# Kernel optimization log

Hardware: AMD Instinct MI355X
Metric: run time of the kernel (lower is better)

## Reference

```python
import jax, jax.numpy as jnp
import numpy as np

HIDDEN = 256
PA = 32          # pairwise_attention_size
PW = 64          # pairwise_size
B, L = 4, 512


def setup_inputs() -> dict:
    key = jax.random.key(0)
    k1, k2, k3, k4, k5, k6 = jax.random.split(key, 6)
    s_in = 1.0 / np.sqrt(HIDDEN)
    s_out = 1.0 / np.sqrt(PA * PA)
    return {
        "hidden_states": jax.random.normal(k1, (B, L, HIDDEN), dtype=jnp.float32),
        "pairwise_states": jax.random.normal(k2, (B, L, L, PW), dtype=jnp.float32),
        "W_in": jax.random.uniform(k3, (PA, HIDDEN), jnp.float32, -s_in, s_in),
        "b_in": jax.random.uniform(k4, (PA,), jnp.float32, -s_in, s_in),
        "W_out": jax.random.uniform(k5, (PW, PA * PA), jnp.float32, -s_out, s_out),
        "b_out": jax.random.uniform(k6, (PW,), jnp.float32, -s_out, s_out),
    }


def reference(hidden_states, pairwise_states, W_in, b_in, W_out, b_out):
    # in_proj: [B, L, H] -> [B, L, PA]
    h = jnp.einsum("blh,ph->blp", hidden_states, W_in) + b_in
    # Original math: triangle[b,i,j,p,q] = h[b,j,p] * h[b,i,q], flattened (p major)
    # then out_proj. Algebraically reorder to avoid the [B,L,L,PA^2] intermediate:
    # out[b,i,j,o] = sum_{p,q} W_out[o, p*PA+q] * h[b,j,p] * h[b,i,q] + b_out[o]
    Wr = W_out.reshape(W_out.shape[0], PA, PA)  # [O, p, q]
    t = jnp.einsum("bjp,opq->bjoq", h, Wr)       # small: [B, L, O, PA]
    out = jnp.einsum("bjoq,biq->bijo", t, h) + b_out
    return out + pairwise_states
```

## Files before the change

kernel.cpp:

```cpp
#include <hip/hip_runtime.h>

#define BB  4
#define LL  512
#define HID 256
#define PAi 32
#define OO  64

using bf16x8 = __attribute__((ext_vector_type(8))) short;
using f32x4  = __attribute__((ext_vector_type(4))) float;

__device__ inline ushort f2bf(float x) {
    union { float f; unsigned u; } v; v.f = x;
    unsigned r = (v.u + 0x7fff + ((v.u >> 16) & 1)) >> 16;
    return (ushort)r;
}

__device__ inline void barrier_lds() {
    asm volatile("s_waitcnt lgkmcnt(0)" ::: "memory");
    __builtin_amdgcn_s_barrier();
}

__global__ __launch_bounds__(256) void k_in(const float* __restrict__ hidden,
                                            const float* __restrict__ W_in,
                                            const float* __restrict__ b_in,
                                            float* __restrict__ h,
                                            ushort* __restrict__ hb) {
    __shared__ float4 hid[8 * 64];
    const int tid  = threadIdx.x;
    const int row0 = blockIdx.x * 8;
    const float4* src = (const float4*)(hidden + (size_t)row0 * HID);
    hid[tid]       = src[tid];
    hid[tid + 256] = src[tid + 256];
    __syncthreads();
    const int p = tid & 31;
    const int r = tid >> 5;
    const float4* w = (const float4*)(W_in + (size_t)p * HID);
    float acc = 0.f;
#pragma unroll
    for (int k = 0; k < 64; ++k) {
        float4 hv = hid[r * 64 + k];
        float4 wv = w[k];
        acc += hv.x * wv.x + hv.y * wv.y + hv.z * wv.z + hv.w * wv.w;
    }
    const float val = acc + b_in[p];
    h[(size_t)(row0 + r) * PAi + p]  = val;
    hb[(size_t)(row0 + r) * PAi + p] = f2bf(val);
}

#define RMID 16
__global__ __launch_bounds__(256) void k_mid(const float* __restrict__ h,
                                             const float* __restrict__ W_out,
                                             ushort* __restrict__ t) {
    __shared__ __attribute__((aligned(16))) float hst[PAi][RMID];
    const int tid  = threadIdx.x;
    const int row0 = blockIdx.x * RMID;
    for (int s = tid; s < RMID * PAi; s += 256) {
        const int r = s >> 5, p = s & 31;
        hst[p][r] = h[(size_t)(row0 + r) * PAi + p];
    }
    __syncthreads();
    const int qg = tid & 7;
    const int o1 = tid >> 3;
    const float4* W4 = (const float4*)W_out;
    float4 accA[RMID], accB[RMID];
#pragma unroll
    for (int r = 0; r < RMID; ++r) {
        accA[r] = float4{0, 0, 0, 0};
        accB[r] = float4{0, 0, 0, 0};
    }
#pragma unroll 2
    for (int p = 0; p < PAi; ++p) {
        const float4 wa = W4[(o1 * PAi + p) * 8 + qg];
        const float4 wb = W4[((o1 + 32) * PAi + p) * 8 + qg];
#pragma unroll
        for (int r4 = 0; r4 < RMID / 4; ++r4) {
            const float4 h4 = *(const float4*)&hst[p][r4 * 4];
            const float hr[4] = {h4.x, h4.y, h4.z, h4.w};
#pragma unroll
            for (int e = 0; e < 4; ++e) {
                const int r = r4 * 4 + e;
                accA[r].x += hr[e] * wa.x; accA[r].y += hr[e] * wa.y;
                accA[r].z += hr[e] * wa.z; accA[r].w += hr[e] * wa.w;
                accB[r].x += hr[e] * wb.x; accB[r].y += hr[e] * wb.y;
                accB[r].z += hr[e] * wb.z; accB[r].w += hr[e] * wb.w;
            }
        }
    }
#pragma unroll
    for (int r = 0; r < RMID; ++r) {
        ushort4 ua, ub;
        ua.x = f2bf(accA[r].x); ua.y = f2bf(accA[r].y); ua.z = f2bf(accA[r].z); ua.w = f2bf(accA[r].w);
        ub.x = f2bf(accB[r].x); ub.y = f2bf(accB[r].y); ub.z = f2bf(accB[r].z); ub.w = f2bf(accB[r].w);
        ushort* dst = t + (size_t)(row0 + r) * OO * PAi;
        *(ushort4*)(dst + (o1 * 8 + qg) * 4)        = ua;
        *(ushort4*)(dst + ((o1 + 32) * 8 + qg) * 4) = ub;
    }
}

#define WJO  256
#define NIT2 (LL / 32)
#define LSTR 260
__global__ __launch_bounds__(256, 4) void k_out(const ushort* __restrict__ t,
                                                const ushort* __restrict__ hb,
                                                const float* __restrict__ pw,
                                                const float* __restrict__ b_out,
                                                float* __restrict__ out) {
    __shared__ float sA[16 * LSTR];
    __shared__ float sB[16 * LSTR];
    const int tid   = threadIdx.x;
    const int lane  = tid & 63;
    const int wave  = tid >> 6;
    const int b     = blockIdx.z;
    const int ibase = blockIdx.y * (LL / 2);
    const int jo0   = blockIdx.x * WJO;
    const int l15   = lane & 15;
    const int g     = lane >> 4;

    bf16x8 tf[4];
    {
        const ushort* tb0 = t + ((size_t)b * LL * OO + jo0 + wave * 64 + l15) * PAi + g * 8;
#pragma unroll
        for (int tt = 0; tt < 4; ++tt)
            tf[tt] = *(const bf16x8*)(tb0 + (size_t)tt * (16 * PAi));
    }
    const f32x4 bo4 = *(const f32x4*)(b_out + ((lane * 4) & 63));

    auto loadH = [&](int it) -> bf16x8 {
        return *(const bf16x8*)(hb + ((size_t)(b * LL + ibase + it * 16 + l15)) * PAi + g * 8);
    };
    auto loadP = [&](int it, f32x4* pv) {
#pragma unroll
        for (int rr = 0; rr < 4; ++rr)
            pv[rr] = *(const f32x4*)(pw + ((size_t)(b * LL + ibase + it * 16 + wave * 4 + rr)) * (LL * OO)
                                       + jo0 + lane * 4);
    };
    auto mfmaS = [&](const bf16x8 hfi, float* sbuf) {
#pragma unroll
        for (int tt = 0; tt < 4; ++tt) {
            f32x4 z = {0.f, 0.f, 0.f, 0.f};
            f32x4 a = __builtin_amdgcn_mfma_f32_16x16x32_bf16(tf[tt], hfi, z, 0, 0, 0);
            *(f32x4*)&sbuf[l15 * LSTR + wave * 64 + tt * 16 + g * 4] = a;
        }
    };
    auto cons = [&](int it, const f32x4* pv, const float* sbuf) {
#pragma unroll
        for (int rr = 0; rr < 4; ++rr) {
            const f32x4 a4 = *(const f32x4*)&sbuf[(wave * 4 + rr) * LSTR + lane * 4];
            f32x4 res = a4 + bo4 + pv[rr];
            __builtin_nontemporal_store(res,
                (f32x4*)(out + ((size_t)(b * LL + ibase + it * 16 + wave * 4 + rr)) * (LL * OO)
                             + jo0 + lane * 4));
        }
    };

    bf16x8 hfA = loadH(0), hfB = loadH(1);
    f32x4  pvA[4], pvB[4];
    loadP(0, pvA); loadP(1, pvB);

    mfmaS(hfA, sA);
    barrier_lds();

    for (int k = 0; k < NIT2; k += 2) {
        mfmaS(hfB, sB);
        cons(k, pvA, sA);
        if (k + 2 < NIT2) { hfA = loadH(k + 2); loadP(k + 2, pvA); }
        barrier_lds();
        if (k + 2 < NIT2) mfmaS(hfA, sA);
        cons(k + 1, pvB, sB);
        if (k + 3 < NIT2) { hfB = loadH(k + 3); loadP(k + 3, pvB); }
        barrier_lds();
    }
}

extern "C" void kernel_launch(void* const* d_in, const int* in_sizes, int n_in,
                              void* d_out, int out_size, void* d_ws, size_t ws_size,
                              hipStream_t stream) {
    const float* hidden = (const float*)d_in[0];
    const float* pw     = (const float*)d_in[1];
    const float* W_in   = (const float*)d_in[2];
    const float* b_in   = (const float*)d_in[3];
    const float* W_out  = (const float*)d_in[4];
    const float* b_out  = (const float*)d_in[5];
    float* out = (float*)d_out;

    float*  h  = (float*)d_ws;
    ushort* hb = (ushort*)(h + (size_t)BB * LL * PAi);
    ushort* tb = hb + (size_t)BB * LL * PAi;

    k_in <<<dim3(BB * LL / 8), 256, 0, stream>>>(hidden, W_in, b_in, h, hb);
    k_mid<<<dim3(BB * LL / RMID), 256, 0, stream>>>(h, W_out, tb);
    k_out<<<dim3(LL * OO / WJO, 2, BB), 256, 0, stream>>>(tb, hb, pw, b_out, out);
}
```

Before: 112.2 us.

## Reshape k_out tiles to wider jo span and fewer i rows per block

Each k_out block now covers 1024 output columns in four 256-wide chunks over 64 i rows, instead of 256 columns over 256 rows; the grid keeps the same number of blocks. The main loop becomes a fully unrolled 16-step schedule with one barrier per step. pairwise_states loads are prefetched only one step ahead, alternating between two LDS buffers. The aim is to shorten the per-block serial loop and cut loop overhead. In exchange each thread holds four times as many t fragments in registers, and the prefetch distance is shallower, which could expose more memory latency in this bandwidth-bound kernel.

```diff
diff --git a/kernel.cpp b/kernel.cpp
--- a/kernel.cpp
+++ b/kernel.cpp
@@ -97,8 +97,7 @@
     }
 }
 
-#define WJO  256
-#define NIT2 (LL / 32)
+#define WJO  1024
 #define LSTR 260
 __global__ __launch_bounds__(256, 4) void k_out(const ushort* __restrict__ t,
                                                 const ushort* __restrict__ hb,
@@ -111,64 +110,68 @@
     const int lane  = tid & 63;
     const int wave  = tid >> 6;
     const int b     = blockIdx.z;
-    const int ibase = blockIdx.y * (LL / 2);
+    const int ibase = blockIdx.y * 64;
     const int jo0   = blockIdx.x * WJO;
     const int l15   = lane & 15;
     const int g     = lane >> 4;
 
-    bf16x8 tf[4];
+    bf16x8 tf[16];
     {
         const ushort* tb0 = t + ((size_t)b * LL * OO + jo0 + wave * 64 + l15) * PAi + g * 8;
 #pragma unroll
-        for (int tt = 0; tt < 4; ++tt)
-            tf[tt] = *(const bf16x8*)(tb0 + (size_t)tt * (16 * PAi));
+        for (int cc = 0; cc < 4; ++cc)
+#pragma unroll
+            for (int tt = 0; tt < 4; ++tt)
+                tf[cc * 4 + tt] = *(const bf16x8*)(tb0 + (size_t)(cc * 256 + tt * 16) * PAi);
     }
     const f32x4 bo4 = *(const f32x4*)(b_out + ((lane * 4) & 63));
 
     auto loadH = [&](int it) -> bf16x8 {
         return *(const bf16x8*)(hb + ((size_t)(b * LL + ibase + it * 16 + l15)) * PAi + g * 8);
     };
-    auto loadP = [&](int it, f32x4* pv) {
+    auto loadP = [&](int it, int cc, f32x4* pv) {
 #pragma unroll
         for (int rr = 0; rr < 4; ++rr)
-            pv[rr] = *(const f32x4*)(pw + ((size_t)(b * LL + ibase + it * 16 + wave * 4 + rr)) * (LL * OO)
-                                       + jo0 + lane * 4);
+            pv[rr] = *(const f32x4*)(pw +
+                ((size_t)(b * LL + ibase + it * 16 + wave * 4 + rr)) * (LL * OO)
+                + jo0 + cc * 256 + lane * 4);
     };
-    auto mfmaS = [&](const bf16x8 hfi, float* sbuf) {
+    auto mfmaS = [&](int cc, const bf16x8 hfi, float* sbuf) {
 #pragma unroll
         for (int tt = 0; tt < 4; ++tt) {
             f32x4 z = {0.f, 0.f, 0.f, 0.f};
-            f32x4 a = __builtin_amdgcn_mfma_f32_16x16x32_bf16(tf[tt], hfi, z, 0, 0, 0);
+            f32x4 a = __builtin_amdgcn_mfma_f32_16x16x32_bf16(tf[cc * 4 + tt], hfi, z, 0, 0, 0);
             *(f32x4*)&sbuf[l15 * LSTR + wave * 64 + tt * 16 + g * 4] = a;
         }
     };
-    auto cons = [&](int it, const f32x4* pv, const float* sbuf) {
+    auto cons = [&](int it, int cc, const f32x4* pv, const float* sbuf) {
 #pragma unroll
         for (int rr = 0; rr < 4; ++rr) {
             const f32x4 a4 = *(const f32x4*)&sbuf[(wave * 4 + rr) * LSTR + lane * 4];
             f32x4 res = a4 + bo4 + pv[rr];
-            __builtin_nontemporal_store(res,
-                (f32x4*)(out + ((size_t)(b * LL + ibase + it * 16 + wave * 4 + rr)) * (LL * OO)
-                             + jo0 + lane * 4));
+            __builtin_nontemporal_store(res, (f32x4*)(out +
+                ((size_t)(b * LL + ibase + it * 16 + wave * 4 + rr)) * (LL * OO)
+                + jo0 + cc * 256 + lane * 4));
         }
     };
 
-    bf16x8 hfA = loadH(0), hfB = loadH(1);
-    f32x4  pvA[4], pvB[4];
-    loadP(0, pvA); loadP(1, pvB);
+    bf16x8 hf[4];
+    hf[0] = loadH(0);
+    hf[1] = loadH(1);
+    f32x4 pv[2][4];
+    loadP(0, 0, pv[0]);
 
-    mfmaS(hfA, sA);
-    barrier_lds();
-
-    for (int k = 0; k < NIT2; k += 2) {
-        mfmaS(hfB, sB);
-        cons(k, pvA, sA);
-        if (k + 2 < NIT2) { hfA = loadH(k + 2); loadP(k + 2, pvA); }
-        barrier_lds();
-        if (k + 2 < NIT2) mfmaS(hfA, sA);
-        cons(k + 1, pvB, sB);
-        if (k + 3 < NIT2) { hfB = loadH(k + 3); loadP(k + 3, pvB); }
-        barrier_lds();
+#pragma unroll
+    for (int it = 0; it < 4; ++it) {
+#pragma unroll
+        for (int cc = 0; cc < 4; ++cc) {
+            const int s = it * 4 + cc;
+            if (cc == 0 && it < 2) hf[it + 2] = loadH(it + 2);
+            if (s + 1 < 16) loadP((s + 1) >> 2, (s + 1) & 3, pv[(s + 1) & 1]);
+            mfmaS(cc, hf[it], (s & 1) ? sB : sA);
+            barrier_lds();
+            cons(it, cc, pv[s & 1], (s & 1) ? sB : sA);
+        }
     }
 }
 
@@ -189,5 +192,5 @@
 
     k_in <<<dim3(BB * LL / 8), 256, 0, stream>>>(hidden, W_in, b_in, h, hb);
     k_mid<<<dim3(BB * LL / RMID), 256, 0, stream>>>(h, W_out, tb);
-    k_out<<<dim3(LL * OO / WJO, 2, BB), 256, 0, stream>>>(tb, hb, pw, b_out, out);
+    k_out<<<dim3(LL * OO / WJO, LL / 64, BB), 256, 0, stream>>>(tb, hb, pw, b_out, out);
 }
```

After: 161.9 us. 44.4% more time.
